# Kernel optimization log

Measured on AMD Instinct MI355X. Metric: run time of the kernel, lower is better.

## Reference

```python
import jax, jax.numpy as jnp
import numpy as np

LOG2_HASHMAP_SIZE = 19
HASHMAP_MASK = np.uint32((1 << LOG2_HASHMAP_SIZE) - 1)
# num_mf_layers=4 -> mf_layer_indices=[2,5,8,11] of the 12-level geometric
# resolution list between base=16 and finest=512
RESOLUTIONS = (30, 80, 210, 512)
PRIMES = (np.uint32(1), np.uint32(11614769), np.uint32(2654435761))
N_POINTS = 2_000_000
N_FEATS = 2

# 8 corner offsets of a 3D voxel, shape [8, 3]
CORNER_OFFSETS = jnp.array([[i, j, k] for i in (0, 1) for j in (0, 1) for k in (0, 1)], dtype=jnp.int32)


def _hash3(coords):
    # coords: [..., 3] int32 grid coordinates -> [...] int32 hash index
    c = coords.astype(jnp.uint32)
    h = (c[..., 0] * PRIMES[0]) ^ (c[..., 1] * PRIMES[1]) ^ (c[..., 2] * PRIMES[2])
    return (h & HASHMAP_MASK).astype(jnp.int32)


def setup_inputs() -> dict:
    key = jax.random.key(0)
    k1, k2 = jax.random.split(key)
    # points inside the unit bounding box
    x = jax.random.uniform(k1, (N_POINTS, 3), dtype=jnp.float32)
    # 4 hash tables, init U(-1e-4, 1e-4) as in nn.init.uniform_
    tables = jax.random.uniform(k2, (len(RESOLUTIONS), 1 << LOG2_HASHMAP_SIZE, N_FEATS),
                                minval=-1e-4, maxval=1e-4, dtype=jnp.float32)
    return {"x": x, "tables": tables}


def reference(x, tables):
    # x: [N, 3] in [0, 1]; tables: [L, 2^19, F]
    outs = []
    for li, res in enumerate(RESOLUTIONS):
        scaled = x * jnp.float32(res)          # [N, 3]
        bottom = jnp.floor(scaled)             # voxel min vertex
        t = scaled - bottom                    # relative position in voxel, [N, 3]
        corners = bottom.astype(jnp.int32)[:, None, :] + CORNER_OFFSETS[None]  # [N, 8, 3]
        idx = _hash3(corners)                  # [N, 8]
        emb = tables[li][idx]                  # gather corner embeddings, [N, 8, F]
        # trilinear weights: prod over dims of (t if offset==1 else 1-t)
        w = jnp.where(CORNER_OFFSETS[None].astype(bool), t[:, None, :], 1.0 - t[:, None, :]).prod(axis=-1)  # [N, 8]
        outs.append(jnp.einsum('nc,ncf->nf', w, emb))  # [N, F]
    return jnp.concatenate(outs, axis=-1)  # [N, L*F] = [N, 8]
```

## Files before the change

### kernel.cpp

```cpp
#include <hip/hip_runtime.h>
#include <hip/hip_fp16.h>
#include <stdint.h>

#define LOG2_HASHMAP_SIZE 19
#define HASHMAP_SIZE (1u << LOG2_HASHMAP_SIZE)
#define HASHMAP_MASK (HASHMAP_SIZE - 1u)
#define N_LEVELS 4

#define R0 31
#define DENSE0_N (R0 * R0 * R0)
#define DENSE0_BYTES (DENSE0_N * 4)

#define R1 81
#define ZQ1 41
#define D1_N (R1 * R1 * R1)
#define ZP_N (R1 * ZQ1 * R1)
#define ZP_BYTES ((size_t)ZP_N * 8)

typedef float v4f __attribute__((ext_vector_type(4)));
typedef unsigned int v2u __attribute__((ext_vector_type(2)));

__device__ __forceinline__ uint32_t hash3(uint32_t ix, uint32_t iy, uint32_t iz) {
    return (ix ^ (iy * 11614769u) ^ (iz * 2654435761u)) & HASHMAP_MASK;
}

__device__ __forceinline__ float2 h2f(uint32_t p) {
    return __half22float2(*(const __half2*)&p);
}
__device__ __forceinline__ uint32_t f2h(float a, float b) {
    const __half2 p = __floats2half2_rn(a, b);
    return *(const uint32_t*)&p;
}

__device__ __forceinline__ uint4 load16u(const uint2* p) {
    uint4 v;
    __builtin_memcpy(&v, p, 16);
    return v;
}

__device__ __forceinline__ float2 level_embed_p(float px, float py, float pz,
                                                const float* __restrict__ tables,
                                                int li, float r)
{
    const uint32_t P1 = 11614769u;
    const uint32_t P2 = 2654435761u;

    const float sx = px * r, sy = py * r, sz = pz * r;
    const float bx = floorf(sx), by = floorf(sy), bz = floorf(sz);
    const float tx = sx - bx, ty = sy - by, tz = sz - bz;
    const float ux = 1.0f - tx, uy = 1.0f - ty, uz = 1.0f - tz;

    const uint32_t ix = (uint32_t)(int)bx;
    const uint32_t iy = (uint32_t)(int)by;
    const uint32_t iz = (uint32_t)(int)bz;

    const uint32_t hy0 = iy * P1, hy1 = (iy + 1u) * P1;
    const uint32_t hz0 = iz * P2, hz1 = (iz + 1u) * P2;

    uint32_t S[4];
    float W[4];
    S[0] = hy0 ^ hz0;  W[0] = uy * uz;
    S[1] = hy0 ^ hz1;  W[1] = uy * tz;
    S[2] = hy1 ^ hz0;  W[2] = ty * uz;
    S[3] = hy1 ^ hz1;  W[3] = ty * tz;

    const float* tab = tables + (size_t)li * HASHMAP_SIZE * 2;
    const float2* __restrict__ tab2 = (const float2*)tab;

    float f0 = 0.0f, f1 = 0.0f;
    #pragma unroll
    for (int c = 0; c < 4; ++c) {
        const uint32_t h0 = (ix ^ S[c]) & HASHMAP_MASK;
        const uint32_t h1 = ((ix + 1u) ^ S[c]) & HASHMAP_MASK;
        const float2 e0 = tab2[h0];
        const float2 e1 = tab2[h1];
        f0 += W[c] * (ux * e0.x + tx * e1.x);
        f1 += W[c] * (ux * e0.y + tx * e1.y);
    }
    return make_float2(f0, f1);
}

__device__ __forceinline__ float2 level_embed_h16(float px, float py, float pz,
                                                  const uint32_t* __restrict__ t16,
                                                  float r)
{
    const uint32_t P1 = 11614769u;
    const uint32_t P2 = 2654435761u;

    const float sx = px * r, sy = py * r, sz = pz * r;
    const float bx = floorf(sx), by = floorf(sy), bz = floorf(sz);
    const float tx = sx - bx, ty = sy - by, tz = sz - bz;
    const float ux = 1.0f - tx, uy = 1.0f - ty, uz = 1.0f - tz;

    const uint32_t ix = (uint32_t)(int)bx;
    const uint32_t iy = (uint32_t)(int)by;
    const uint32_t iz = (uint32_t)(int)bz;

    const uint32_t hy0 = iy * P1, hy1 = (iy + 1u) * P1;
    const uint32_t hz0 = iz * P2, hz1 = (iz + 1u) * P2;

    uint32_t S[4];
    float W[4];
    S[0] = hy0 ^ hz0;  W[0] = uy * uz;
    S[1] = hy0 ^ hz1;  W[1] = uy * tz;
    S[2] = hy1 ^ hz0;  W[2] = ty * uz;
    S[3] = hy1 ^ hz1;  W[3] = ty * tz;

    float f0 = 0.0f, f1 = 0.0f;
    if ((ix & 1u) == 0u) {
        #pragma unroll
        for (int c = 0; c < 4; ++c) {
            const uint32_t h0 = (ix ^ S[c]) & HASHMAP_MASK;
            const uint2 v = ((const uint2*)t16)[h0 >> 1];
            const uint32_t p0 = (h0 & 1u) ? v.y : v.x;
            const uint32_t p1 = (h0 & 1u) ? v.x : v.y;
            const float2 e0 = h2f(p0);
            const float2 e1 = h2f(p1);
            f0 += W[c] * (ux * e0.x + tx * e1.x);
            f1 += W[c] * (ux * e0.y + tx * e1.y);
        }
    } else {
        #pragma unroll
        for (int c = 0; c < 4; ++c) {
            const uint32_t h0 = (ix ^ S[c]) & HASHMAP_MASK;
            const uint32_t h1 = ((ix + 1u) ^ S[c]) & HASHMAP_MASK;
            const float2 e0 = h2f(t16[h0]);
            const float2 e1 = h2f(t16[h1]);
            f0 += W[c] * (ux * e0.x + tx * e1.x);
            f1 += W[c] * (ux * e0.y + tx * e1.y);
        }
    }
    return make_float2(f0, f1);
}

__device__ __forceinline__ float2 level1_zp(float px, float py, float pz,
                                            const uint2* __restrict__ zp)
{
    const float sx = px * 80.0f, sy = py * 80.0f, sz = pz * 80.0f;
    const float bx = floorf(sx), by = floorf(sy), bz = floorf(sz);
    const float tx = sx - bx, ty = sy - by, tz = sz - bz;
    const float ux = 1.0f - tx, uy = 1.0f - ty, uz = 1.0f - tz;
    const int ix = (int)bx, iy = (int)by, iz = (int)bz;

    const int zq = iz >> 1;
    const size_t rowx0 = ((size_t)ix * ZQ1 + zq) * R1 + iy;
    const size_t rowx1 = rowx0 + (size_t)ZQ1 * R1;

    float2 a00, a01, a10, a11;
    float2 b00, b01, b10, b11;
    if ((iz & 1) == 0) {
        const uint4 a = load16u(zp + rowx0);
        const uint4 b = load16u(zp + rowx1);
        a00 = h2f(a.x); a01 = h2f(a.y); a10 = h2f(a.z); a11 = h2f(a.w);
        b00 = h2f(b.x); b01 = h2f(b.y); b10 = h2f(b.z); b11 = h2f(b.w);
    } else {
        const uint4 a0 = load16u(zp + rowx0);
        const uint4 a1 = load16u(zp + rowx0 + R1);
        const uint4 b0 = load16u(zp + rowx1);
        const uint4 b1 = load16u(zp + rowx1 + R1);
        a00 = h2f(a0.y); a01 = h2f(a1.x); a10 = h2f(a0.w); a11 = h2f(a1.z);
        b00 = h2f(b0.y); b01 = h2f(b1.x); b10 = h2f(b0.w); b11 = h2f(b1.z);
    }

    const float w00 = ux * uy, w10 = ux * ty, wx0 = tx * uy, wx1 = tx * ty;
    const float f0 = w00 * (uz * a00.x + tz * a01.x)
                   + w10 * (uz * a10.x + tz * a11.x)
                   + wx0 * (uz * b00.x + tz * b01.x)
                   + wx1 * (uz * b10.x + tz * b11.x);
    const float f1 = w00 * (uz * a00.y + tz * a01.y)
                   + w10 * (uz * a10.y + tz * a11.y)
                   + wx0 * (uz * b00.y + tz * b01.y)
                   + wx1 * (uz * b10.y + tz * b11.y);
    return make_float2(f0, f1);
}

__global__ __launch_bounds__(256) void convert_fp16(
    const float* __restrict__ tables, uint32_t* __restrict__ t16)
{
    const int i = blockIdx.x * blockDim.x + threadIdx.x;
    if (i >= 2 * (int)HASHMAP_SIZE) return;
    const float2 e = ((const float2*)tables)[2 * HASHMAP_SIZE + i];
    t16[i] = f2h(e.x, e.y);
}

__global__ __launch_bounds__(256) void build_dense0(
    const float* __restrict__ tables, uint32_t* __restrict__ dense0)
{
    const int v = blockIdx.x * blockDim.x + threadIdx.x;
    if (v >= DENSE0_N) return;
    const int vx = v / (R0 * R0);
    const int rem = v - vx * (R0 * R0);
    const int vy = rem / R0;
    const int vz = rem - vy * R0;
    const uint32_t h = hash3((uint32_t)vx, (uint32_t)vy, (uint32_t)vz);
    const float2 e = ((const float2*)tables)[h];
    dense0[v] = f2h(e.x, e.y);
}

__global__ __launch_bounds__(256) void build_dense1(
    const float* __restrict__ tables, uint32_t* __restrict__ d1)
{
    const int v = blockIdx.x * blockDim.x + threadIdx.x;
    if (v >= D1_N) return;
    const int vx = v / (R1 * R1);
    const int rem = v - vx * (R1 * R1);
    const int vy = rem / R1;
    const int vz = rem - vy * R1;
    const uint32_t h = hash3((uint32_t)vx, (uint32_t)vy, (uint32_t)vz);
    const float2 e = ((const float2*)tables)[HASHMAP_SIZE + h];
    d1[v] = f2h(e.x, e.y);
}

__global__ __launch_bounds__(256) void expand_zp(
    const uint32_t* __restrict__ d1, uint2* __restrict__ zp)
{
    const int t = blockIdx.x * blockDim.x + threadIdx.x;
    if (t >= ZP_N) return;
    const int x  = t / (ZQ1 * R1);
    int rem = t - x * (ZQ1 * R1);
    const int zq = rem / R1;
    const int y  = rem - zq * R1;
    const int z0 = 2 * zq;
    const int z1 = min(z0 + 1, R1 - 1);
    const uint32_t* base = d1 + ((size_t)x * R1 + y) * R1;
    uint2 q;
    q.x = base[z0];
    q.y = base[z1];
    zp[t] = q;
}

__global__ __launch_bounds__(256) void passA_kernel(
    const float* __restrict__ x, const uint2* __restrict__ zp,
    const uint32_t* __restrict__ t16_l2, unsigned int* __restrict__ wsA, int n)
{
    const int i = blockIdx.x * blockDim.x + threadIdx.x;
    if (i >= n) return;
    const float px = __builtin_nontemporal_load(x + 3 * (size_t)i + 0);
    const float py = __builtin_nontemporal_load(x + 3 * (size_t)i + 1);
    const float pz = __builtin_nontemporal_load(x + 3 * (size_t)i + 2);

    const float2 e1 = level1_zp(px, py, pz, zp);
    const float2 e2 = level_embed_h16(px, py, pz, t16_l2, 210.0f);

    v2u o = {f2h(e1.x, e1.y), f2h(e2.x, e2.y)};
    __builtin_nontemporal_store(o, (v2u*)wsA + i);
}

extern __shared__ uint32_t s_dense[];

__global__ __launch_bounds__(1024) void final16_kernel(
    const float* __restrict__ x, const uint32_t* __restrict__ t16_l3,
    const uint32_t* __restrict__ dense0,
    const unsigned int* __restrict__ wsA, float* __restrict__ out, int n)
{
    for (int i = threadIdx.x; i < DENSE0_N; i += 1024)
        s_dense[i] = dense0[i];
    __syncthreads();

    const size_t stride = (size_t)gridDim.x * 1024;
    for (size_t i = (size_t)blockIdx.x * 1024 + threadIdx.x; i < (size_t)n; i += stride) {
        const float px = __builtin_nontemporal_load(x + 3 * i + 0);
        const float py = __builtin_nontemporal_load(x + 3 * i + 1);
        const float pz = __builtin_nontemporal_load(x + 3 * i + 2);

        const float2 e3 = level_embed_h16(px, py, pz, t16_l3, 512.0f);

        const float sx = px * 30.0f, sy = py * 30.0f, sz = pz * 30.0f;
        const float bx = floorf(sx), by = floorf(sy), bz = floorf(sz);
        const float tx = sx - bx, ty = sy - by, tz = sz - bz;
        const float uxv = 1.0f - tx, uyv = 1.0f - ty, uzv = 1.0f - tz;
        const int ix = (int)bx, iy = (int)by, iz = (int)bz;
        const int lin = (ix * R0 + iy) * R0 + iz;

        float f0 = 0.0f, f1 = 0.0f;
        #pragma unroll
        for (int dx = 0; dx < 2; ++dx) {
            const float wx = dx ? tx : uxv;
            #pragma unroll
            for (int dy = 0; dy < 2; ++dy) {
                const float wxy = wx * (dy ? ty : uyv);
                const int base = lin + (dx * R0 + dy) * R0;
                const float2 c0 = h2f(s_dense[base]);
                const float2 c1 = h2f(s_dense[base + 1]);
                f0 += wxy * (uzv * c0.x + tz * c1.x);
                f1 += wxy * (uzv * c0.y + tz * c1.y);
            }
        }

        const v2u w = __builtin_nontemporal_load((const v2u*)wsA + i);
        const float2 e1 = h2f(w.x);
        const float2 e2 = h2f(w.y);

        v4f* op = (v4f*)(out + 8 * i);
        v4f lo = {f0, f1, e1.x, e1.y};
        v4f hi = {e2.x, e2.y, e3.x, e3.y};
        __builtin_nontemporal_store(lo, op);
        __builtin_nontemporal_store(hi, op + 1);
    }
}

__global__ __launch_bounds__(256) void pass_direct_kernel(
    const float* __restrict__ x, const float* __restrict__ tables,
    float* __restrict__ out, int li, float r, int n)
{
    const int i = blockIdx.x * blockDim.x + threadIdx.x;
    if (i >= n) return;
    const float px = x[3 * (size_t)i + 0];
    const float py = x[3 * (size_t)i + 1];
    const float pz = x[3 * (size_t)i + 2];
    const float2 e = level_embed_p(px, py, pz, tables, li, r);
    float2* op = (float2*)(out + 8 * (size_t)i + 2 * li);
    *op = e;
}

extern "C" void kernel_launch(void* const* d_in, const int* in_sizes, int n_in,
                              void* d_out, int out_size, void* d_ws, size_t ws_size,
                              hipStream_t stream) {
    const float* x = (const float*)d_in[0];
    const float* tables = (const float*)d_in[1];
    float* out = (float*)d_out;
    const int n = in_sizes[0] / 3;

    const size_t t16_bytes = 2 * (size_t)HASHMAP_SIZE * 4;
    const size_t off_zp    = t16_bytes;
    const size_t off_d1    = off_zp + ZP_BYTES;
    const size_t off_d0    = off_d1 + (size_t)D1_N * 4;
    const size_t off_wsA   = off_d0 + DENSE0_BYTES;
    const size_t ws_needed = off_wsA + (size_t)n * 8;

    bool fused_ok = (ws_size >= ws_needed);
    if (fused_ok) {
        static int attr_ok = -1;
        if (attr_ok < 0) {
            attr_ok = (hipFuncSetAttribute(
                           reinterpret_cast<const void*>(final16_kernel),
                           hipFuncAttributeMaxDynamicSharedMemorySize,
                           DENSE0_BYTES) == hipSuccess) ? 1 : 0;
        }
        fused_ok = (attr_ok == 1);
    }

    if (fused_ok) {
        char* wsb = (char*)d_ws;
        uint32_t* t16    = (uint32_t*)wsb;
        uint2*    zp     = (uint2*)(wsb + off_zp);
        uint32_t* d1     = (uint32_t*)(wsb + off_d1);
        uint32_t* dense0 = (uint32_t*)(wsb + off_d0);
        unsigned int* wsA = (unsigned int*)(wsb + off_wsA);

        convert_fp16<<<(2 * HASHMAP_SIZE + 255) / 256, 256, 0, stream>>>(tables, t16);
        build_dense0<<<(DENSE0_N + 255) / 256, 256, 0, stream>>>(tables, dense0);
        build_dense1<<<(D1_N + 255) / 256, 256, 0, stream>>>(tables, d1);
        expand_zp<<<(ZP_N + 255) / 256, 256, 0, stream>>>(d1, zp);

        const int block = 256;
        const int grid = (n + block - 1) / block;
        passA_kernel<<<grid, block, 0, stream>>>(x, zp, t16, wsA, n);
        final16_kernel<<<256, 1024, DENSE0_BYTES, stream>>>(
            x, t16 + HASHMAP_SIZE, dense0, wsA, out, n);
    } else {
        const float res[N_LEVELS] = {30.0f, 80.0f, 210.0f, 512.0f};
        const int block = 256;
        const int grid = (n + block - 1) / block;
        for (int li = 0; li < N_LEVELS; ++li) {
            pass_direct_kernel<<<grid, block, 0, stream>>>(
                x, tables, out, li, res[li], n);
        }
    }
}
```

Baseline: 250.1 us.

## Fuse setup kernels and merge level passes into one main kernel

Merges the four table-preparation kernels into a single setup kernel and builds the z-paired level-1 table straight from the hash table, dropping the intermediate dense1 buffer. The passA and final kernels become one kernel that computes all four levels per point, so the fp16 intermediate buffer is no longer written and read back and x is read once instead of twice. The fused kernel uses more registers and issues more scattered gathers per thread, which may reduce occupancy with 1024-thread blocks. The grid also goes from 256 to 512 blocks.

```diff
diff --git a/kernel.cpp b/kernel.cpp
--- a/kernel.cpp
+++ b/kernel.cpp
@@ -13,12 +13,12 @@
 
 #define R1 81
 #define ZQ1 41
-#define D1_N (R1 * R1 * R1)
 #define ZP_N (R1 * ZQ1 * R1)
 #define ZP_BYTES ((size_t)ZP_N * 8)
 
+#define CONV_N (2 * (int)HASHMAP_SIZE)
+
 typedef float v4f __attribute__((ext_vector_type(4)));
-typedef unsigned int v2u __attribute__((ext_vector_type(2)));
 
 __device__ __forceinline__ uint32_t hash3(uint32_t ix, uint32_t iy, uint32_t iz) {
     return (ix ^ (iy * 11614769u) ^ (iz * 2654435761u)) & HASHMAP_MASK;
@@ -174,84 +174,58 @@
     return make_float2(f0, f1);
 }
 
-__global__ __launch_bounds__(256) void convert_fp16(
-    const float* __restrict__ tables, uint32_t* __restrict__ t16)
-{
-    const int i = blockIdx.x * blockDim.x + threadIdx.x;
-    if (i >= 2 * (int)HASHMAP_SIZE) return;
-    const float2 e = ((const float2*)tables)[2 * HASHMAP_SIZE + i];
-    t16[i] = f2h(e.x, e.y);
-}
-
-__global__ __launch_bounds__(256) void build_dense0(
-    const float* __restrict__ tables, uint32_t* __restrict__ dense0)
-{
-    const int v = blockIdx.x * blockDim.x + threadIdx.x;
-    if (v >= DENSE0_N) return;
-    const int vx = v / (R0 * R0);
-    const int rem = v - vx * (R0 * R0);
-    const int vy = rem / R0;
-    const int vz = rem - vy * R0;
-    const uint32_t h = hash3((uint32_t)vx, (uint32_t)vy, (uint32_t)vz);
-    const float2 e = ((const float2*)tables)[h];
-    dense0[v] = f2h(e.x, e.y);
-}
-
-__global__ __launch_bounds__(256) void build_dense1(
-    const float* __restrict__ tables, uint32_t* __restrict__ d1)
-{
-    const int v = blockIdx.x * blockDim.x + threadIdx.x;
-    if (v >= D1_N) return;
-    const int vx = v / (R1 * R1);
-    const int rem = v - vx * (R1 * R1);
-    const int vy = rem / R1;
-    const int vz = rem - vy * R1;
-    const uint32_t h = hash3((uint32_t)vx, (uint32_t)vy, (uint32_t)vz);
-    const float2 e = ((const float2*)tables)[HASHMAP_SIZE + h];
-    d1[v] = f2h(e.x, e.y);
-}
-
-__global__ __launch_bounds__(256) void expand_zp(
-    const uint32_t* __restrict__ d1, uint2* __restrict__ zp)
-{
-    const int t = blockIdx.x * blockDim.x + threadIdx.x;
-    if (t >= ZP_N) return;
-    const int x  = t / (ZQ1 * R1);
-    int rem = t - x * (ZQ1 * R1);
-    const int zq = rem / R1;
-    const int y  = rem - zq * R1;
-    const int z0 = 2 * zq;
-    const int z1 = min(z0 + 1, R1 - 1);
-    const uint32_t* base = d1 + ((size_t)x * R1 + y) * R1;
-    uint2 q;
-    q.x = base[z0];
-    q.y = base[z1];
-    zp[t] = q;
-}
-
-__global__ __launch_bounds__(256) void passA_kernel(
-    const float* __restrict__ x, const uint2* __restrict__ zp,
-    const uint32_t* __restrict__ t16_l2, unsigned int* __restrict__ wsA, int n)
-{
-    const int i = blockIdx.x * blockDim.x + threadIdx.x;
-    if (i >= n) return;
-    const float px = __builtin_nontemporal_load(x + 3 * (size_t)i + 0);
-    const float py = __builtin_nontemporal_load(x + 3 * (size_t)i + 1);
-    const float pz = __builtin_nontemporal_load(x + 3 * (size_t)i + 2);
-
-    const float2 e1 = level1_zp(px, py, pz, zp);
-    const float2 e2 = level_embed_h16(px, py, pz, t16_l2, 210.0f);
-
-    v2u o = {f2h(e1.x, e1.y), f2h(e2.x, e2.y)};
-    __builtin_nontemporal_store(o, (v2u*)wsA + i);
+__global__ __launch_bounds__(256) void setup_all(
+    const float* __restrict__ tables,
+    uint32_t* __restrict__ t16,
+    uint32_t* __restrict__ dense0,
+    uint2* __restrict__ zp)
+{
+    int i = blockIdx.x * blockDim.x + threadIdx.x;
+
+    if (i < CONV_N) {
+        const float2 e = ((const float2*)tables)[2 * HASHMAP_SIZE + i];
+        t16[i] = f2h(e.x, e.y);
+        return;
+    }
+    i -= CONV_N;
+
+    if (i < DENSE0_N) {
+        const int vx = i / (R0 * R0);
+        const int rem = i - vx * (R0 * R0);
+        const int vy = rem / R0;
+        const int vz = rem - vy * R0;
+        const uint32_t h = hash3((uint32_t)vx, (uint32_t)vy, (uint32_t)vz);
+        const float2 e = ((const float2*)tables)[h];
+        dense0[i] = f2h(e.x, e.y);
+        return;
+    }
+    i -= DENSE0_N;
+
+    if (i < ZP_N) {
+        const int x  = i / (ZQ1 * R1);
+        int rem = i - x * (ZQ1 * R1);
+        const int zq = rem / R1;
+        const int y  = rem - zq * R1;
+        const int z0 = 2 * zq;
+        const int z1 = min(z0 + 1, R1 - 1);
+        const float2* tab1 = (const float2*)tables + HASHMAP_SIZE;
+        const float2 e0 = tab1[hash3((uint32_t)x, (uint32_t)y, (uint32_t)z0)];
+        const float2 e1 = tab1[hash3((uint32_t)x, (uint32_t)y, (uint32_t)z1)];
+        uint2 q;
+        q.x = f2h(e0.x, e0.y);
+        q.y = f2h(e1.x, e1.y);
+        zp[i] = q;
+    }
 }
 
 extern __shared__ uint32_t s_dense[];
 
-__global__ __launch_bounds__(1024) void final16_kernel(
-    const float* __restrict__ x, const uint32_t* __restrict__ t16_l3,
+__global__ __launch_bounds__(1024) void fused_all(
+    const float* __restrict__ x,
+    const uint32_t* __restrict__ t16,
+    const uint2* __restrict__ zp,
     const uint32_t* __restrict__ dense0,
-    const unsigned int* __restrict__ wsA, float* __restrict__ out, int n)
+    float* __restrict__ out, int n)
 {
     for (int i = threadIdx.x; i < DENSE0_N; i += 1024)
         s_dense[i] = dense0[i];
@@ -263,7 +237,9 @@
         const float py = __builtin_nontemporal_load(x + 3 * i + 1);
         const float pz = __builtin_nontemporal_load(x + 3 * i + 2);
 
-        const float2 e3 = level_embed_h16(px, py, pz, t16_l3, 512.0f);
+        const float2 e3 = level_embed_h16(px, py, pz, t16 + HASHMAP_SIZE, 512.0f);
+        const float2 e2 = level_embed_h16(px, py, pz, t16, 210.0f);
+        const float2 e1 = level1_zp(px, py, pz, zp);
 
         const float sx = px * 30.0f, sy = py * 30.0f, sz = pz * 30.0f;
         const float bx = floorf(sx), by = floorf(sy), bz = floorf(sz);
@@ -287,10 +263,6 @@
             }
         }
 
-        const v2u w = __builtin_nontemporal_load((const v2u*)wsA + i);
-        const float2 e1 = h2f(w.x);
-        const float2 e2 = h2f(w.y);
-
         v4f* op = (v4f*)(out + 8 * i);
         v4f lo = {f0, f1, e1.x, e1.y};
         v4f hi = {e2.x, e2.y, e3.x, e3.y};
@@ -323,17 +295,15 @@
 
     const size_t t16_bytes = 2 * (size_t)HASHMAP_SIZE * 4;
     const size_t off_zp    = t16_bytes;
-    const size_t off_d1    = off_zp + ZP_BYTES;
-    const size_t off_d0    = off_d1 + (size_t)D1_N * 4;
-    const size_t off_wsA   = off_d0 + DENSE0_BYTES;
-    const size_t ws_needed = off_wsA + (size_t)n * 8;
+    const size_t off_d0    = off_zp + ZP_BYTES;
+    const size_t ws_needed = off_d0 + DENSE0_BYTES;
 
     bool fused_ok = (ws_size >= ws_needed);
     if (fused_ok) {
         static int attr_ok = -1;
         if (attr_ok < 0) {
             attr_ok = (hipFuncSetAttribute(
-                           reinterpret_cast<const void*>(final16_kernel),
+                           reinterpret_cast<const void*>(fused_all),
                            hipFuncAttributeMaxDynamicSharedMemorySize,
                            DENSE0_BYTES) == hipSuccess) ? 1 : 0;
         }
@@ -344,20 +314,14 @@
         char* wsb = (char*)d_ws;
         uint32_t* t16    = (uint32_t*)wsb;
         uint2*    zp     = (uint2*)(wsb + off_zp);
-        uint32_t* d1     = (uint32_t*)(wsb + off_d1);
         uint32_t* dense0 = (uint32_t*)(wsb + off_d0);
-        unsigned int* wsA = (unsigned int*)(wsb + off_wsA);
-
-        convert_fp16<<<(2 * HASHMAP_SIZE + 255) / 256, 256, 0, stream>>>(tables, t16);
-        build_dense0<<<(DENSE0_N + 255) / 256, 256, 0, stream>>>(tables, dense0);
-        build_dense1<<<(D1_N + 255) / 256, 256, 0, stream>>>(tables, d1);
-        expand_zp<<<(ZP_N + 255) / 256, 256, 0, stream>>>(d1, zp);
-
-        const int block = 256;
-        const int grid = (n + block - 1) / block;
-        passA_kernel<<<grid, block, 0, stream>>>(x, zp, t16, wsA, n);
-        final16_kernel<<<256, 1024, DENSE0_BYTES, stream>>>(
-            x, t16 + HASHMAP_SIZE, dense0, wsA, out, n);
+
+        const int setup_total = CONV_N + DENSE0_N + ZP_N;
+        setup_all<<<(setup_total + 255) / 256, 256, 0, stream>>>(
+            tables, t16, dense0, zp);
+
+        fused_all<<<512, 1024, DENSE0_BYTES, stream>>>(
+            x, t16, zp, dense0, out, n);
     } else {
         const float res[N_LEVELS] = {30.0f, 80.0f, 210.0f, 512.0f};
         const int block = 256;
```

After: 275.2 us. 10.0% more time.
